# Kernel optimization log

Hardware: AMD Instinct MI355X
Metric: run time of the kernel (lower is better)

The kernel has to match this reference:

```python
import jax, jax.numpy as jnp
import numpy as np

B, C_IN, C_OUT, K, H, W = 32, 128, 256, 3, 56, 56
STRIDE, PAD = 1, 1


def setup_inputs() -> dict:
    key = jax.random.key(0)
    kx, kw, kb = jax.random.split(key, 3)
    x = jax.random.normal(kx, (B, C_IN, H, W), dtype=jnp.float32)
    weight = jax.random.normal(kw, (C_OUT, C_IN, K, K), dtype=jnp.float32)
    bias = jax.random.normal(kb, (C_OUT,), dtype=jnp.float32)
    return {"x": x, "weight": weight, "bias": bias}


def reference(x, weight, bias):
    # Binarize weights to {-1, 0, +1} exactly like torch.sign
    w_bin = jnp.sign(weight)
    out = jax.lax.conv_general_dilated(
        x, w_bin,
        window_strides=(STRIDE, STRIDE),
        padding=[(PAD, PAD), (PAD, PAD)],
        dimension_numbers=("NCHW", "OIHW", "NCHW"),
    )
    return out + bias[None, :, None, None]
```

## Files before the change

kernel.cpp:

```cpp
#include <hip/hip_runtime.h>
#include <cstdint>
#include <cstddef>

typedef _Float16 f16;
typedef _Float16 f16x4 __attribute__((ext_vector_type(4)));
typedef _Float16 f16x8 __attribute__((ext_vector_type(8)));
typedef float    f32x4 __attribute__((ext_vector_type(4)));

#define CIN    128
#define COUT   256
#define HH     56
#define WW     56
#define HW     3136
#define PPDIM  3364
#define XPLANE (PPDIM*CIN)

__global__ __launch_bounds__(256) void xpad_kernel(const float* __restrict__ x,
                                                   f16* __restrict__ xp) {
  int bid  = blockIdx.x;
  int cblk = bid & 1;
  int h    = (bid >> 1) % HH;
  int b    = bid / (2*HH);
  int c0   = cblk * 64;
  __shared__ f16 tile[WW][73];
  for (int idx = threadIdx.x; idx < 64*WW; idx += 256) {
    int cl = idx / WW, w = idx % WW;
    float v = x[((size_t)(b*CIN + c0 + cl)*HH + h)*WW + w];
    tile[w][cl] = (f16)v;
  }
  __syncthreads();
  f16* op = xp + (size_t)b*XPLANE + (size_t)((h+1)*58 + 1)*CIN + c0;
  for (int idx = threadIdx.x; idx < WW*16; idx += 256) {
    int w = idx >> 4, c4 = (idx & 15) << 2;
    f16x4 t = { tile[w][c4], tile[w][c4+1], tile[w][c4+2], tile[w][c4+3] };
    *(f16x4*)(op + (size_t)w*CIN + c4) = t;
  }
}

__global__ __launch_bounds__(256) void wprep_kernel(const float* __restrict__ w,
                                                    f16* __restrict__ wt) {
  int t = blockIdx.x*256 + threadIdx.x;
  int s  = t >> 13;
  int r  = t & 8191;
  int co = r >> 5;
  int cl = r & 31;
  int kidx = s >> 2;
  int c  = ((s & 3) << 5) + cl;
  float v = w[(size_t)co*1152 + c*9 + kidx];
  wt[t] = (f16)((v > 0.f) ? 1.f : (v < 0.f ? -1.f : 0.f));
}

__global__ __launch_bounds__(512, 2) void bconv_main(
    const f16* __restrict__ xp, const f16* __restrict__ wt,
    const float* __restrict__ bias, float* __restrict__ out) {
  __shared__ __align__(16) f16 Alds[128][40];
  __shared__ __align__(16) f16 Blds[256][40];
  const int tid = threadIdx.x;
  const int p0  = blockIdx.x * 128;

  const int px_s = tid >> 2;
  const int part = tid & 3;
  const int p_g  = p0 + px_s;
  const int b_s  = p_g / HW;
  const int pos  = p_g % HW;
  const int hs   = pos / WW;
  const int ws_  = pos % WW;
  const long xbase = (long)b_s*XPLANE + (long)((hs+1)*58 + ws_ + 1)*CIN + part*8;

  const int wave = tid >> 6, lane = tid & 63;
  const int wpx = wave >> 2;
  const int wco = wave & 3;
  const int l15 = lane & 15, l4 = lane >> 4;

  f32x4 acc[4][4];
  #pragma unroll
  for (int i = 0; i < 4; ++i)
    #pragma unroll
    for (int j = 0; j < 4; ++j)
      acc[i][j] = (f32x4){0.f, 0.f, 0.f, 0.f};

  #pragma unroll 1
  for (int kidx = 0; kidx < 9; ++kidx) {
    const int dh = kidx/3 - 1, dw = kidx - (kidx/3)*3 - 1;
    const f16* xsrc = xp + (xbase + (long)(dh*58 + dw)*CIN);
    #pragma unroll 1
    for (int cb = 0; cb < 4; ++cb) {
      const int s = kidx*4 + cb;
      f16x8 av = *(const f16x8*)(xsrc + cb*32);
      const f16* wsrc = wt + (size_t)s*8192 + tid*16;
      f16x8 bv0 = *(const f16x8*)(wsrc);
      f16x8 bv1 = *(const f16x8*)(wsrc + 8);
      *(f16x8*)&Alds[px_s][part*8] = av;
      const int co_s = tid >> 1;
      const int cs   = (tid & 1) << 4;
      *(f16x8*)&Blds[co_s][cs]     = bv0;
      *(f16x8*)&Blds[co_s][cs + 8] = bv1;
      __syncthreads();
      f16x8 xf[4], wf[4];
      #pragma unroll
      for (int j = 0; j < 4; ++j)
        xf[j] = *(const f16x8*)&Alds[wpx*64 + j*16 + l15][l4*8];
      #pragma unroll
      for (int i = 0; i < 4; ++i)
        wf[i] = *(const f16x8*)&Blds[wco*64 + i*16 + l15][l4*8];
      #pragma unroll
      for (int i = 0; i < 4; ++i)
        #pragma unroll
        for (int j = 0; j < 4; ++j)
          acc[i][j] = __builtin_amdgcn_mfma_f32_16x16x32_f16(wf[i], xf[j], acc[i][j], 0, 0, 0);
      __syncthreads();
    }
  }

  #pragma unroll
  for (int j = 0; j < 4; ++j) {
    const int pg = p0 + wpx*64 + j*16 + l15;
    const int bb = pg / HW;
    const int pr = pg % HW;
    float* ob = out + (size_t)bb*(COUT*HW) + pr;
    #pragma unroll
    for (int i = 0; i < 4; ++i) {
      const int cb2 = wco*64 + i*16 + l4*4;
      #pragma unroll
      for (int r = 0; r < 4; ++r) {
        const int co = cb2 + r;
        ob[(size_t)co*HW] = acc[i][j][r] + bias[co];
      }
    }
  }
}

extern "C" void kernel_launch(void* const* d_in, const int* in_sizes, int n_in,
                              void* d_out, int out_size, void* d_ws, size_t ws_size,
                              hipStream_t stream) {
  const float* x    = (const float*)d_in[0];
  const float* w    = (const float*)d_in[1];
  const float* bias = (const float*)d_in[2];
  float* out = (float*)d_out;

  f16* xp = (f16*)d_ws;
  f16* wt = xp + (size_t)32*XPLANE;

  hipMemsetAsync(d_ws, 0, (size_t)32*XPLANE*sizeof(f16), stream);
  xpad_kernel<<<3584, 256, 0, stream>>>(x, xp);
  wprep_kernel<<<1152, 256, 0, stream>>>(w, wt);
  bconv_main<<<784, 512, 0, stream>>>(xp, wt, bias, out);
}
```

Before: 243.4 us.

## Load conv tiles directly to LDS with K=64 swizzled stages and fused padding

The main conv kernel now stages A and B tiles with global_load_lds (direct global-to-LDS copies) instead of going through registers. Each stage covers 64 channels instead of 32, which halves the number of barrier pairs, and the weight and LDS layouts use an XOR swizzle to avoid bank conflicts. The padding kernel now writes whole padded rows, including zero borders, so the separate memset is dropped, and it reads the input with vectorized loads. The trade-off is larger LDS use per block and the loss of the 2-blocks-per-CU launch bound, which may lower occupancy.

```diff
diff --git a/kernel.cpp b/kernel.cpp
--- a/kernel.cpp
+++ b/kernel.cpp
@@ -15,116 +15,148 @@
 #define PPDIM  3364
 #define XPLANE (PPDIM*CIN)
 
+__device__ __forceinline__ void gload16(const void* g, void* l) {
+  __builtin_amdgcn_global_load_lds((const __attribute__((address_space(1))) unsigned int*)g,
+                                   (__attribute__((address_space(3))) unsigned int*)l,
+                                   16, 0, 0);
+}
+
 __global__ __launch_bounds__(256) void xpad_kernel(const float* __restrict__ x,
                                                    f16* __restrict__ xp) {
-  int bid  = blockIdx.x;
-  int cblk = bid & 1;
-  int h    = (bid >> 1) % HH;
-  int b    = bid / (2*HH);
-  int c0   = cblk * 64;
-  __shared__ f16 tile[WW][73];
-  for (int idx = threadIdx.x; idx < 64*WW; idx += 256) {
-    int cl = idx / WW, w = idx % WW;
-    float v = x[((size_t)(b*CIN + c0 + cl)*HH + h)*WW + w];
-    tile[w][cl] = (f16)v;
+  const int bid = blockIdx.x;
+  const int pr  = bid % 58;
+  const int b   = bid / 58;
+  const int tid = threadIdx.x;
+  __shared__ f16 tile[128 * 65];
+
+  const bool interior = (pr >= 1) && (pr <= 56);
+  if (interior) {
+    const int h = pr - 1;
+    #pragma unroll
+    for (int it = 0; it < 7; ++it) {
+      int i  = it * 256 + tid;
+      int c  = i / 14;
+      int wq = i - c * 14;
+      const float* src = x + (((size_t)(b * CIN + c) * HH + h) * WW + wq * 4);
+      f32x4 v = *(const f32x4*)src;
+      f16x4 t = { (f16)v.x, (f16)v.y, (f16)v.z, (f16)v.w };
+      *(f16x4*)&tile[c * 65 + wq * 4] = t;
+    }
   }
   __syncthreads();
-  f16* op = xp + (size_t)b*XPLANE + (size_t)((h+1)*58 + 1)*CIN + c0;
-  for (int idx = threadIdx.x; idx < WW*16; idx += 256) {
-    int w = idx >> 4, c4 = (idx & 15) << 2;
-    f16x4 t = { tile[w][c4], tile[w][c4+1], tile[w][c4+2], tile[w][c4+3] };
-    *(f16x4*)(op + (size_t)w*CIN + c4) = t;
+  f16* orow = xp + (size_t)b * XPLANE + (size_t)pr * 58 * CIN;
+  for (int i = tid; i < 928; i += 256) {
+    int px = i >> 4;
+    int cg = i & 15;
+    f16x8 v = {};
+    if (interior && px >= 1 && px <= 56) {
+      int w = px - 1;
+      #pragma unroll
+      for (int j = 0; j < 8; ++j) v[j] = tile[(cg * 8 + j) * 65 + w];
+    }
+    *(f16x8*)(orow + (size_t)px * CIN + cg * 8) = v;
   }
 }
 
 __global__ __launch_bounds__(256) void wprep_kernel(const float* __restrict__ w,
                                                     f16* __restrict__ wt) {
-  int t = blockIdx.x*256 + threadIdx.x;
-  int s  = t >> 13;
-  int r  = t & 8191;
-  int co = r >> 5;
-  int cl = r & 31;
-  int kidx = s >> 2;
-  int c  = ((s & 3) << 5) + cl;
-  float v = w[(size_t)co*1152 + c*9 + kidx];
+  int t = blockIdx.x * 256 + threadIdx.x;
+  int s     = t >> 14;
+  int hidx  = t & 16383;
+  int co    = hidx >> 6;
+  int khalf = (hidx & 63) ^ ((co & 4) << 2);
+  int kidx  = s >> 1;
+  int c     = ((s & 1) << 6) + khalf;
+  float v = w[(size_t)co * 1152 + c * 9 + kidx];
   wt[t] = (f16)((v > 0.f) ? 1.f : (v < 0.f ? -1.f : 0.f));
 }
 
-__global__ __launch_bounds__(512, 2) void bconv_main(
+__global__ __launch_bounds__(512) void bconv_main(
     const f16* __restrict__ xp, const f16* __restrict__ wt,
     const float* __restrict__ bias, float* __restrict__ out) {
-  __shared__ __align__(16) f16 Alds[128][40];
-  __shared__ __align__(16) f16 Blds[256][40];
+  __shared__ __align__(16) f16 Alds[128 * 64];
+  __shared__ __align__(16) f16 Blds[256 * 64];
   const int tid = threadIdx.x;
   const int p0  = blockIdx.x * 128;
 
-  const int px_s = tid >> 2;
-  const int part = tid & 3;
-  const int p_g  = p0 + px_s;
-  const int b_s  = p_g / HW;
-  const int pos  = p_g % HW;
-  const int hs   = pos / WW;
-  const int ws_  = pos % WW;
-  const long xbase = (long)b_s*XPLANE + (long)((hs+1)*58 + ws_ + 1)*CIN + part*8;
+  const int wave = tid >> 6, lane = tid & 63;
+  const int pxl  = tid >> 3;
+  const int kx_s = ((tid & 7) << 4) ^ ((pxl & 4) << 3);
+  const int pga  = p0 + pxl;
+  const int pgb  = pga + 64;
+  const int ba = pga / HW, ra = pga % HW;
+  const int bb = pgb / HW, rb = pgb % HW;
+  const int ha = ra / WW, wa = ra % WW;
+  const int hb = rb / WW, wb = rb % WW;
+  const char* xpB = (const char*)xp;
+  const char* srcA0 = xpB + 2 * ((size_t)ba * XPLANE + (size_t)((ha + 1) * 58 + wa + 1) * CIN) + kx_s;
+  const char* srcA1 = xpB + 2 * ((size_t)bb * XPLANE + (size_t)((hb + 1) * 58 + wb + 1) * CIN) + kx_s;
+  char* AldsB = (char*)Alds;
+  char* BldsB = (char*)Blds;
+  char* dstA0 = AldsB + (wave << 10);
+  char* dstA1 = AldsB + 8192 + (wave << 10);
+  const char* wtB = (const char*)wt + (tid << 4);
+  char* dstB = BldsB + (wave << 10);
 
-  const int wave = tid >> 6, lane = tid & 63;
   const int wpx = wave >> 2;
   const int wco = wave & 3;
   const int l15 = lane & 15, l4 = lane >> 4;
+  const int kxr = (l15 & 4) << 3;
+  const int rA = ((wpx << 6) + l15) << 7;
+  const int rB = ((wco << 6) + l15) << 7;
 
   f32x4 acc[4][4];
   #pragma unroll
   for (int i = 0; i < 4; ++i)
     #pragma unroll
-    for (int j = 0; j < 4; ++j)
-      acc[i][j] = (f32x4){0.f, 0.f, 0.f, 0.f};
+    for (int j = 0; j < 4; ++j) acc[i][j] = (f32x4){0.f, 0.f, 0.f, 0.f};
 
   #pragma unroll 1
-  for (int kidx = 0; kidx < 9; ++kidx) {
-    const int dh = kidx/3 - 1, dw = kidx - (kidx/3)*3 - 1;
-    const f16* xsrc = xp + (xbase + (long)(dh*58 + dw)*CIN);
-    #pragma unroll 1
-    for (int cb = 0; cb < 4; ++cb) {
-      const int s = kidx*4 + cb;
-      f16x8 av = *(const f16x8*)(xsrc + cb*32);
-      const f16* wsrc = wt + (size_t)s*8192 + tid*16;
-      f16x8 bv0 = *(const f16x8*)(wsrc);
-      f16x8 bv1 = *(const f16x8*)(wsrc + 8);
-      *(f16x8*)&Alds[px_s][part*8] = av;
-      const int co_s = tid >> 1;
-      const int cs   = (tid & 1) << 4;
-      *(f16x8*)&Blds[co_s][cs]     = bv0;
-      *(f16x8*)&Blds[co_s][cs + 8] = bv1;
-      __syncthreads();
+  for (int s = 0; s < 18; ++s) {
+    const int kidx = s >> 1, ch = s & 1;
+    const int dh = kidx / 3 - 1, dw = kidx - (kidx / 3) * 3 - 1;
+    const long toff = (long)(dh * 58 + dw) * 256 + ch * 128;
+    gload16(srcA0 + toff, dstA0);
+    gload16(srcA1 + toff, dstA1);
+    const char* ws = wtB + (size_t)s * 32768;
+    gload16(ws,         dstB);
+    gload16(ws + 8192,  dstB + 8192);
+    gload16(ws + 16384, dstB + 16384);
+    gload16(ws + 24576, dstB + 24576);
+    __syncthreads();
+
+    #pragma unroll
+    for (int kk = 0; kk < 2; ++kk) {
+      const int ko = ((kk << 6) + (l4 << 4)) ^ kxr;
       f16x8 xf[4], wf[4];
       #pragma unroll
       for (int j = 0; j < 4; ++j)
-        xf[j] = *(const f16x8*)&Alds[wpx*64 + j*16 + l15][l4*8];
+        xf[j] = *(const f16x8*)(AldsB + rA + (j << 11) + ko);
       #pragma unroll
       for (int i = 0; i < 4; ++i)
-        wf[i] = *(const f16x8*)&Blds[wco*64 + i*16 + l15][l4*8];
+        wf[i] = *(const f16x8*)(BldsB + rB + (i << 11) + ko);
       #pragma unroll
       for (int i = 0; i < 4; ++i)
         #pragma unroll
         for (int j = 0; j < 4; ++j)
           acc[i][j] = __builtin_amdgcn_mfma_f32_16x16x32_f16(wf[i], xf[j], acc[i][j], 0, 0, 0);
-      __syncthreads();
     }
+    __syncthreads();
   }
 
   #pragma unroll
   for (int j = 0; j < 4; ++j) {
-    const int pg = p0 + wpx*64 + j*16 + l15;
-    const int bb = pg / HW;
+    const int pg = p0 + wpx * 64 + j * 16 + l15;
+    const int bo = pg / HW;
     const int pr = pg % HW;
-    float* ob = out + (size_t)bb*(COUT*HW) + pr;
+    float* ob = out + (size_t)bo * (COUT * HW) + pr;
     #pragma unroll
     for (int i = 0; i < 4; ++i) {
-      const int cb2 = wco*64 + i*16 + l4*4;
+      const int cb2 = wco * 64 + i * 16 + l4 * 4;
       #pragma unroll
       for (int r = 0; r < 4; ++r) {
         const int co = cb2 + r;
-        ob[(size_t)co*HW] = acc[i][j][r] + bias[co];
+        ob[(size_t)co * HW] = acc[i][j][r] + bias[co];
       }
     }
   }
@@ -139,10 +171,9 @@
   float* out = (float*)d_out;
 
   f16* xp = (f16*)d_ws;
-  f16* wt = xp + (size_t)32*XPLANE;
+  f16* wt = xp + (size_t)32 * XPLANE;
 
-  hipMemsetAsync(d_ws, 0, (size_t)32*XPLANE*sizeof(f16), stream);
-  xpad_kernel<<<3584, 256, 0, stream>>>(x, xp);
+  xpad_kernel<<<1856, 256, 0, stream>>>(x, xp);
   wprep_kernel<<<1152, 256, 0, stream>>>(w, wt);
   bconv_main<<<784, 512, 0, stream>>>(xp, wt, bias, out);
 }
```

Measured after the change: 207.0 us. 14.9% less time.
